# Kernel optimization log

Hardware: AMD Instinct MI355X
Metric: run time of the kernel (lower is better)

## Reference

```python
import jax, jax.numpy as jnp
import numpy as np

N_NODES = 32768
N_EDGES = 524288
N_FEAT = 256
HID = 256
N_GRAPHS = 64
N_CLASSES = 4
NODES_PER_GRAPH = N_NODES // N_GRAPHS
BN_EPS = 1e-5


def setup_inputs() -> dict:
    key = jax.random.key(0)
    ks = jax.random.split(key, 16)
    x = jax.random.normal(ks[0], (N_NODES, N_FEAT), dtype=jnp.float32)
    edge_index = jax.random.randint(ks[1], (2, N_EDGES), 0, N_NODES, dtype=jnp.int32)
    batch = (jnp.arange(N_NODES, dtype=jnp.int32) // NODES_PER_GRAPH)
    def xavier(k, shape):
        fan_in, fan_out = shape[0], shape[1]
        a = float(np.sqrt(6.0 / (fan_in + fan_out)))
        return jax.random.uniform(k, shape, jnp.float32, -a, a)
    return {
        "x": x, "edge_index": edge_index, "batch": batch,
        "W1": xavier(ks[2], (N_FEAT, HID)), "b1": jnp.zeros((HID,), jnp.float32),
        "g1": jnp.ones((HID,), jnp.float32), "be1": jnp.zeros((HID,), jnp.float32),
        "W2": xavier(ks[3], (HID, HID)), "b2": jnp.zeros((HID,), jnp.float32),
        "g2": jnp.ones((HID,), jnp.float32), "be2": jnp.zeros((HID,), jnp.float32),
        "W_ih": xavier(ks[4], (HID, 4 * HID)), "W_hh": xavier(ks[5], (HID, 4 * HID)),
        "b_ih": jnp.zeros((4 * HID,), jnp.float32), "b_hh": jnp.zeros((4 * HID,), jnp.float32),
        "W_fc": xavier(ks[6], (HID, N_CLASSES)), "b_fc": jnp.zeros((N_CLASSES,), jnp.float32),
    }


def gcn_conv(x, W, b, src, dst):
    # PyG GCNConv: add self-loops, symmetric normalization, aggregate, then bias
    h = x @ W                                   # [N, H]
    deg = jnp.zeros((x.shape[0],), h.dtype).at[dst].add(1.0) + 1.0  # in-deg + self-loop
    dinv = jax.lax.rsqrt(deg)
    coef = dinv[src] * dinv[dst]                # [E]
    msg = h[src] * coef[:, None]                # gather + scale, [E, H]
    agg = jnp.zeros_like(h).at[dst].add(msg)    # scatter-add
    agg = agg + h * (1.0 / deg)[:, None]        # self-loop term (norm = 1/deg)
    return agg + b


def batch_norm(x, gamma, beta):
    mean = jnp.mean(x, axis=0)
    var = jnp.mean(jnp.square(x - mean), axis=0)  # biased, as torch BN training
    return (x - mean) * jax.lax.rsqrt(var + BN_EPS) * gamma + beta


def reference(x, edge_index, batch, W1, b1, g1, be1, W2, b2, g2, be2,
              W_ih, W_hh, b_ih, b_hh, W_fc, b_fc):
    src, dst = edge_index[0], edge_index[1]
    h = jax.nn.relu(batch_norm(gcn_conv(x, W1, b1, src, dst), g1, be1))
    h = jax.nn.relu(batch_norm(gcn_conv(h, W2, b2, src, dst), g2, be2))
    # global mean pool over graphs
    sums = jax.ops.segment_sum(h, batch, num_segments=N_GRAPHS)
    cnts = jax.ops.segment_sum(jnp.ones((h.shape[0],), h.dtype), batch, num_segments=N_GRAPHS)
    pooled = sums / cnts[:, None]               # [G, H]
    # LSTM, seq_len = 1, zero initial state -> single cell step
    h0 = jnp.zeros((N_GRAPHS, HID), h.dtype)
    c0 = jnp.zeros((N_GRAPHS, HID), h.dtype)
    gates = pooled @ W_ih + h0 @ W_hh + b_ih + b_hh  # [G, 4H]
    i, f, g, o = jnp.split(gates, 4, axis=1)
    c1 = jax.nn.sigmoid(f) * c0 + jax.nn.sigmoid(i) * jnp.tanh(g)
    h1 = jax.nn.sigmoid(o) * jnp.tanh(c1)
    logits = h1 @ W_fc + b_fc
    logp = jax.nn.log_softmax(logits, axis=1)
    return (logp, (h1[None], c1[None]))
```

## Files before the change

kernel.cpp:

```cpp
#include <hip/hip_runtime.h>
#include <math.h>

#define N_NODES 32768
#define N_FEAT 256
#define HID 256
#define N_GRAPHS 64
#define NPG 512
#define N_CLASSES 4
#define BN_EPS 1e-5f

typedef __attribute__((ext_vector_type(8))) short bf16x8;
typedef __attribute__((ext_vector_type(4))) float f32x4;

__device__ __forceinline__ ushort f2b(float f) {
    union { float f; uint u; } v; v.f = f;
    uint u = v.u;
    return (ushort)((u + 0x7FFFu + ((u >> 16) & 1u)) >> 16);
}
__device__ __forceinline__ float bflo(uint u) {
    union { uint u; float f; } v; v.u = u << 16;
    return v.f;
}
__device__ __forceinline__ float bfhi(uint u) {
    union { uint u; float f; } v; v.u = u & 0xFFFF0000u;
    return v.f;
}

__global__ void k_count_prep(const int* __restrict__ dst, int* __restrict__ degcnt, int cntB,
                             const float* __restrict__ x, ushort* __restrict__ xb, int xB,
                             const float* __restrict__ W1, const float* __restrict__ W2,
                             ushort* __restrict__ Wt1, ushort* __restrict__ Wt2,
                             uint* __restrict__ csrs, int E) {
    int b = blockIdx.x;
    int t = threadIdx.x;
    if (b < cntB) {
        int e = b * 256 + t;
        if (e < E) atomicAdd(&degcnt[dst[e]], 1);
    } else if (b < cntB + xB) {
        int i = (b - cntB) * 256 + t;
        float4 v0 = *(const float4*)(x + (size_t)i * 8);
        float4 v1 = *(const float4*)(x + (size_t)i * 8 + 4);
        uint4 o;
        o.x = (uint)f2b(v0.x) | ((uint)f2b(v0.y) << 16);
        o.y = (uint)f2b(v0.z) | ((uint)f2b(v0.w) << 16);
        o.z = (uint)f2b(v1.x) | ((uint)f2b(v1.y) << 16);
        o.w = (uint)f2b(v1.z) | ((uint)f2b(v1.w) << 16);
        *(uint4*)(xb + (size_t)i * 8) = o;
    } else if (b < cntB + xB + 512) {
        int wb = b - cntB - xB;
        const float* W = (wb < 256) ? W1 : W2;
        ushort* Wt = (wb < 256) ? Wt1 : Wt2;
        int n = wb & 255;
        Wt[n * 256 + t] = f2b(W[t * 256 + n]);
    } else {
        int i = (b - cntB - xB - 512) * 256 + t;
        uint4 s = make_uint4(N_NODES, N_NODES, N_NODES, N_NODES);
        *(uint4*)(csrs + (size_t)i * 4) = s;
    }
}

__global__ __launch_bounds__(1024) void k_scan_all(const int* __restrict__ degcnt,
                                                   float* __restrict__ dinv,
                                                   int* __restrict__ row_start,
                                                   int* __restrict__ cursor,
                                                   uint* __restrict__ csrs,
                                                   ushort* __restrict__ hs_pad) {
    __shared__ int wsum[16];
    int t = threadIdx.x;
    int base = t * 32;
    int s = 0;
#pragma unroll
    for (int i = 0; i < 32; ++i) {
        int c = degcnt[base + i];
        s += (c + 2) & ~1;
    }
    int lane = t & 63, w = t >> 6;
    int v = s;
    for (int off = 1; off < 64; off <<= 1) {
        int u = __shfl_up(v, off);
        if (lane >= off) v += u;
    }
    if (lane == 63) wsum[w] = v;
    __syncthreads();
    if (t < 16) {
        int x = wsum[t];
        for (int off = 1; off < 16; off <<= 1) {
            int u = __shfl_up(x, off, 16);
            if (t >= off) x += u;
        }
        wsum[t] = x;
    }
    __syncthreads();
    int run = ((w > 0) ? wsum[w - 1] : 0) + v - s;
    for (int i = 0; i < 32; ++i) {
        int n = base + i;
        int c = degcnt[n];
        row_start[n] = run;
        csrs[run] = (uint)n;
        cursor[n] = run + 1;
        dinv[n] = rsqrtf((float)(c + 1));
        run += (c + 2) & ~1;
    }
    if (t == 0) row_start[N_NODES] = wsum[15];
    if (t < 128) ((uint*)hs_pad)[t] = 0;
}

__device__ __forceinline__ void fill_body(int e, const int* __restrict__ src,
                                          const int* __restrict__ dst,
                                          int* __restrict__ cursor, uint* __restrict__ csrs,
                                          int E) {
    if (e >= E) return;
    int d = dst[e];
    int pos = atomicAdd(&cursor[d], 1);
    csrs[pos] = (uint)src[e];
}

__device__ __forceinline__ void gemm_body(int bid, const ushort* __restrict__ A,
                                          const ushort* __restrict__ Bt,
                                          const float* __restrict__ dinv,
                                          ushort* __restrict__ hs) {
    int wid = threadIdx.x >> 6;
    int lane = threadIdx.x & 63;
    int xcd = bid & 7;
    int slot = bid >> 3;
    int cb = slot & 3;
    int pr = xcd + ((slot >> 2) << 3);
    int m0 = pr * 256 + wid * 64;
    int n0 = cb * 64;
    int r = lane & 15;
    int ko = (lane >> 4) * 8;

    const ushort* Ab = A + (size_t)(m0 + r) * 256 + ko;
    const ushort* Bb = Bt + (size_t)(n0 + r) * 256 + ko;

    f32x4 acc[4][4] = {};
#pragma unroll
    for (int ks = 0; ks < 8; ++ks) {
        bf16x8 a[4], b[4];
#pragma unroll
        for (int i = 0; i < 4; ++i) {
            a[i] = *(const bf16x8*)(Ab + i * (16 * 256) + ks * 32);
            b[i] = *(const bf16x8*)(Bb + i * (16 * 256) + ks * 32);
        }
#pragma unroll
        for (int i = 0; i < 4; ++i)
#pragma unroll
            for (int j = 0; j < 4; ++j)
                acc[i][j] = __builtin_amdgcn_mfma_f32_16x16x32_bf16(a[i], b[j], acc[i][j], 0, 0, 0);
    }

    int rr = (lane >> 4) * 4;
    int cc = lane & 15;
#pragma unroll
    for (int i = 0; i < 4; ++i) {
        int row = m0 + i * 16 + rr;
#pragma unroll
        for (int r2 = 0; r2 < 4; ++r2) {
            float dv = dinv[row + r2];
#pragma unroll
            for (int j = 0; j < 4; ++j) {
                int col = n0 + j * 16 + cc;
                hs[(size_t)(row + r2) * 256 + col] = f2b(acc[i][j][r2] * dv);
            }
        }
    }
}

__global__ __launch_bounds__(256) void k_fill_gemm1(const ushort* __restrict__ A,
                                                    const ushort* __restrict__ Bt,
                                                    const float* __restrict__ dinv,
                                                    ushort* __restrict__ hs,
                                                    const int* __restrict__ src,
                                                    const int* __restrict__ dst,
                                                    int* __restrict__ cursor,
                                                    uint* __restrict__ csrs, int E) {
    int b = blockIdx.x;
    if (b < 512) {
        gemm_body(b, A, Bt, dinv, hs);
    } else {
        fill_body((b - 512) * 256 + threadIdx.x, src, dst, cursor, csrs, E);
    }
}

__global__ __launch_bounds__(256) void k_gemm2(const ushort* __restrict__ A,
                                               const ushort* __restrict__ Bt,
                                               const float* __restrict__ dinv,
                                               ushort* __restrict__ hs) {
    gemm_body(blockIdx.x, A, Bt, dinv, hs);
}

__global__ __launch_bounds__(256) void k_agg(const ushort* __restrict__ hs,
                                             const uint* __restrict__ csrs,
                                             const int* __restrict__ row_start,
                                             const float* __restrict__ dinv,
                                             const float* __restrict__ bias,
                                             ushort* __restrict__ aggb) {
    int wid = threadIdx.x >> 6;
    int lane = threadIdx.x & 63;
    int half = lane >> 5;
    int fq = lane & 31;
    int n = blockIdx.x * 4 + wid;

    float dv = dinv[n];
    int base = row_start[n];
    int pairs = (row_start[n + 1] - base) >> 1;

    float a0 = 0.f, a1 = 0.f, a2 = 0.f, a3 = 0.f, a4 = 0.f, a5 = 0.f, a6 = 0.f, a7 = 0.f;

    int t = 0;
    for (; t + 4 <= pairs; t += 4) {
        uint s0 = csrs[base + 2 * t + 0 + half];
        uint s1 = csrs[base + 2 * t + 2 + half];
        uint s2 = csrs[base + 2 * t + 4 + half];
        uint s3 = csrs[base + 2 * t + 6 + half];
        uint4 h0 = *(const uint4*)(hs + (size_t)s0 * 256 + fq * 8);
        uint4 h1 = *(const uint4*)(hs + (size_t)s1 * 256 + fq * 8);
        uint4 h2 = *(const uint4*)(hs + (size_t)s2 * 256 + fq * 8);
        uint4 h3 = *(const uint4*)(hs + (size_t)s3 * 256 + fq * 8);
        a0 += bflo(h0.x) + bflo(h1.x) + bflo(h2.x) + bflo(h3.x);
        a1 += bfhi(h0.x) + bfhi(h1.x) + bfhi(h2.x) + bfhi(h3.x);
        a2 += bflo(h0.y) + bflo(h1.y) + bflo(h2.y) + bflo(h3.y);
        a3 += bfhi(h0.y) + bfhi(h1.y) + bfhi(h2.y) + bfhi(h3.y);
        a4 += bflo(h0.z) + bflo(h1.z) + bflo(h2.z) + bflo(h3.z);
        a5 += bfhi(h0.z) + bfhi(h1.z) + bfhi(h2.z) + bfhi(h3.z);
        a6 += bflo(h0.w) + bflo(h1.w) + bflo(h2.w) + bflo(h3.w);
        a7 += bfhi(h0.w) + bfhi(h1.w) + bfhi(h2.w) + bfhi(h3.w);
    }
    for (; t < pairs; ++t) {
        uint s0 = csrs[base + 2 * t + half];
        uint4 h0 = *(const uint4*)(hs + (size_t)s0 * 256 + fq * 8);
        a0 += bflo(h0.x); a1 += bfhi(h0.x);
        a2 += bflo(h0.y); a3 += bfhi(h0.y);
        a4 += bflo(h0.z); a5 += bfhi(h0.z);
        a6 += bflo(h0.w); a7 += bfhi(h0.w);
    }

    a0 += __shfl_xor(a0, 32); a1 += __shfl_xor(a1, 32);
    a2 += __shfl_xor(a2, 32); a3 += __shfl_xor(a3, 32);
    a4 += __shfl_xor(a4, 32); a5 += __shfl_xor(a5, 32);
    a6 += __shfl_xor(a6, 32); a7 += __shfl_xor(a7, 32);

    if (half == 0) {
        float4 b0 = *(const float4*)&bias[fq * 8];
        float4 b1 = *(const float4*)&bias[fq * 8 + 4];
        float o0 = a0 * dv + b0.x, o1 = a1 * dv + b0.y;
        float o2 = a2 * dv + b0.z, o3 = a3 * dv + b0.w;
        float o4 = a4 * dv + b1.x, o5 = a5 * dv + b1.y;
        float o6 = a6 * dv + b1.z, o7 = a7 * dv + b1.w;
        uint4 ov;
        ov.x = (uint)f2b(o0) | ((uint)f2b(o1) << 16);
        ov.y = (uint)f2b(o2) | ((uint)f2b(o3) << 16);
        ov.z = (uint)f2b(o4) | ((uint)f2b(o5) << 16);
        ov.w = (uint)f2b(o6) | ((uint)f2b(o7) << 16);
        *(uint4*)(aggb + (size_t)n * HID + fq * 8) = ov;
    }
}

__global__ __launch_bounds__(256) void k_bn_stats(const ushort* __restrict__ aggb,
                                                  float* __restrict__ bnsum,
                                                  float* __restrict__ bnsq) {
    int t = threadIdx.x;
    int fq = t & 31;
    int rg = t >> 5;
    int r0 = blockIdx.x * 128 + rg * 16;

    float s[8] = {}, q[8] = {};
    for (int r = 0; r < 16; ++r) {
        uint4 v = *(const uint4*)(aggb + (size_t)(r0 + r) * HID + fq * 8);
        float f0 = bflo(v.x), f1 = bfhi(v.x), f2 = bflo(v.y), f3 = bfhi(v.y);
        float f4 = bflo(v.z), f5 = bfhi(v.z), f6 = bflo(v.w), f7 = bfhi(v.w);
        s[0] += f0; q[0] += f0 * f0;  s[1] += f1; q[1] += f1 * f1;
        s[2] += f2; q[2] += f2 * f2;  s[3] += f3; q[3] += f3 * f3;
        s[4] += f4; q[4] += f4 * f4;  s[5] += f5; q[5] += f5 * f5;
        s[6] += f6; q[6] += f6 * f6;  s[7] += f7; q[7] += f7 * f7;
    }

    __shared__ float red[8][32][16];
#pragma unroll
    for (int i = 0; i < 8; ++i) {
        red[rg][fq][i] = s[i];
        red[rg][fq][8 + i] = q[i];
    }
    __syncthreads();
    int fq2 = t & 31;
    int vg = t >> 5;
#pragma unroll
    for (int k = 0; k < 2; ++k) {
        int v = vg * 2 + k;
        float acc = 0.f;
#pragma unroll
        for (int rgi = 0; rgi < 8; ++rgi) acc += red[rgi][fq2][v];
        float* dstp = (v < 8) ? bnsum : bnsq;
        atomicAdd(&dstp[fq2 * 8 + (v & 7)], acc);
    }
}

__global__ void k_bn_apply_b(const ushort* __restrict__ x, const float* __restrict__ bnsum,
                             const float* __restrict__ bnsq, const float* __restrict__ gamma,
                             const float* __restrict__ beta, ushort* __restrict__ out) {
    int i = blockIdx.x * 256 + threadIdx.x;
    if (i >= N_NODES * HID / 4) return;
    int f = (i & 63) * 4;
    const float invN = 1.0f / (float)N_NODES;
    uint2 v = *(const uint2*)(x + (size_t)i * 4);
    float vv[4] = {bflo(v.x), bfhi(v.x), bflo(v.y), bfhi(v.y)};
    float r[4];
#pragma unroll
    for (int qq = 0; qq < 4; ++qq) {
        float mean = bnsum[f + qq] * invN;
        float var = bnsq[f + qq] * invN - mean * mean;
        float t = (vv[qq] - mean) * rsqrtf(var + BN_EPS) * gamma[f + qq] + beta[f + qq];
        r[qq] = t > 0.0f ? t : 0.0f;
    }
    uint2 o;
    o.x = (uint)f2b(r[0]) | ((uint)f2b(r[1]) << 16);
    o.y = (uint)f2b(r[2]) | ((uint)f2b(r[3]) << 16);
    *(uint2*)(out + (size_t)i * 4) = o;
}

__global__ __launch_bounds__(256) void k_bn_pool(const ushort* __restrict__ aggb,
                                                 const float* __restrict__ bnsum,
                                                 const float* __restrict__ bnsq,
                                                 const float* __restrict__ gamma,
                                                 const float* __restrict__ beta,
                                                 float* __restrict__ pooled) {
    int g = blockIdx.x >> 4;
    int blk = blockIdx.x & 15;
    int f = threadIdx.x;
    const float invN = 1.0f / (float)N_NODES;
    float mean = bnsum[f] * invN;
    float var = bnsq[f] * invN - mean * mean;
    float sc = rsqrtf(var + BN_EPS) * gamma[f];
    float sh = beta[f] - mean * sc;
    int r0 = g * NPG + blk * 32;
    float s = 0.0f;
#pragma unroll 4
    for (int r = 0; r < 32; ++r) {
        float v = bflo((uint)aggb[(size_t)(r0 + r) * HID + f]) * sc + sh;
        s += v > 0.0f ? v : 0.0f;
    }
    atomicAdd(&pooled[g * HID + f], s);
}

__global__ __launch_bounds__(256) void k_head(const float* __restrict__ pooled,
                                              const float* __restrict__ W_ih,
                                              const float* __restrict__ b_ih,
                                              const float* __restrict__ b_hh,
                                              const float* __restrict__ W_fc,
                                              const float* __restrict__ b_fc,
                                              float* __restrict__ out) {
    __shared__ float p[HID];
    __shared__ float lsum[N_CLASSES][256];
    __shared__ float logits[N_CLASSES];
    int g = blockIdx.x, j = threadIdx.x;
    p[j] = pooled[g * HID + j] * (1.0f / (float)NPG);
    __syncthreads();

    float gi = 0.f, gf = 0.f, gg = 0.f, go = 0.f;
#pragma unroll 4
    for (int k = 0; k < HID; ++k) {
        float pk = p[k];
        const float* w = &W_ih[(size_t)k * (4 * HID) + j];
        gi += pk * w[0];
        gf += pk * w[HID];
        gg += pk * w[2 * HID];
        go += pk * w[3 * HID];
    }
    gi += b_ih[j] + b_hh[j];
    gf += b_ih[HID + j] + b_hh[HID + j];
    gg += b_ih[2 * HID + j] + b_hh[2 * HID + j];
    go += b_ih[3 * HID + j] + b_hh[3 * HID + j];
    (void)gf;

    float si = 1.f / (1.f + expf(-gi));
    float so = 1.f / (1.f + expf(-go));
    float c1 = si * tanhf(gg);
    float h1 = so * tanhf(c1);

    out[N_GRAPHS * N_CLASSES + g * HID + j] = h1;
    out[N_GRAPHS * N_CLASSES + N_GRAPHS * HID + g * HID + j] = c1;

#pragma unroll
    for (int c = 0; c < N_CLASSES; ++c)
        lsum[c][j] = h1 * W_fc[j * N_CLASSES + c];
    __syncthreads();
    for (int s = 128; s > 0; s >>= 1) {
        if (j < s) {
#pragma unroll
            for (int c = 0; c < N_CLASSES; ++c)
                lsum[c][j] += lsum[c][j + s];
        }
        __syncthreads();
    }
    if (j < N_CLASSES) logits[j] = lsum[j][0] + b_fc[j];
    __syncthreads();
    if (j < N_CLASSES) {
        float m = fmaxf(fmaxf(logits[0], logits[1]), fmaxf(logits[2], logits[3]));
        float lse = m + logf(expf(logits[0] - m) + expf(logits[1] - m) +
                             expf(logits[2] - m) + expf(logits[3] - m));
        out[g * N_CLASSES + j] = logits[j] - lse;
    }
}

extern "C" void kernel_launch(void* const* d_in, const int* in_sizes, int n_in,
                              void* d_out, int out_size, void* d_ws, size_t ws_size,
                              hipStream_t stream) {
    const float* x    = (const float*)d_in[0];
    const int*   ei   = (const int*)d_in[1];
    const float* W1   = (const float*)d_in[3];
    const float* b1   = (const float*)d_in[4];
    const float* g1   = (const float*)d_in[5];
    const float* be1  = (const float*)d_in[6];
    const float* W2   = (const float*)d_in[7];
    const float* b2   = (const float*)d_in[8];
    const float* g2   = (const float*)d_in[9];
    const float* be2  = (const float*)d_in[10];
    const float* W_ih = (const float*)d_in[11];
    const float* b_ih = (const float*)d_in[13];
    const float* b_hh = (const float*)d_in[14];
    const float* W_fc = (const float*)d_in[15];
    const float* b_fc = (const float*)d_in[16];
    float* out = (float*)d_out;

    int E = in_sizes[1] / 2;
    const int* src = ei;
    const int* dst = ei + E;

    const size_t MAT = (size_t)N_NODES * HID;
    size_t SZ = ((size_t)E + 2 * N_NODES + 1023) & ~(size_t)1023;

    ushort* aggb = (ushort*)d_ws;
    ushort* xb   = aggb + MAT;
    ushort* hs   = xb + MAT;
    ushort* Wt1  = hs + MAT + 256;
    ushort* Wt2  = Wt1 + 65536;
    float*  dinv = (float*)(Wt2 + 65536);
    int*    row_start = (int*)(dinv + N_NODES);
    int*    cursor    = row_start + N_NODES + 2;
    uint*   csrs      = (uint*)(cursor + N_NODES);
    int*    degcnt = (int*)(csrs + SZ);
    float*  bn1sum = (float*)(degcnt + N_NODES);
    float*  bn1sq  = bn1sum + HID;
    float*  bn2sum = bn1sq + HID;
    float*  bn2sq  = bn2sum + HID;
    float*  pooled = bn2sq + HID;
    size_t zeroBytes = (size_t)N_NODES * 4 + 4 * HID * 4 + (size_t)N_GRAPHS * HID * 4;

    dim3 blk(256);
    int edgeBlocks = (E + 255) / 256;
    int n8blk = (int)(MAT / 8 / 256);
    int sentB = (int)(SZ / 1024);
    int vec4Blocks = (int)(MAT / 4 / 256);
    int aggBlocks = N_NODES / 4;

    hipMemsetAsync(degcnt, 0, zeroBytes, stream);

    k_count_prep<<<edgeBlocks + n8blk + 512 + sentB, blk, 0, stream>>>(
        dst, degcnt, edgeBlocks, x, xb, n8blk, W1, W2, Wt1, Wt2, csrs, E);
    k_scan_all<<<1, dim3(1024), 0, stream>>>(degcnt, dinv, row_start, cursor, csrs,
                                             hs + MAT);

    k_fill_gemm1<<<512 + edgeBlocks, blk, 0, stream>>>(xb, Wt1, dinv, hs,
                                                       src, dst, cursor, csrs, E);
    k_agg<<<aggBlocks, blk, 0, stream>>>(hs, csrs, row_start, dinv, b1, aggb);
    k_bn_stats<<<N_NODES / 128, blk, 0, stream>>>(aggb, bn1sum, bn1sq);
    k_bn_apply_b<<<vec4Blocks, blk, 0, stream>>>(aggb, bn1sum, bn1sq, g1, be1, xb);

    k_gemm2<<<512, blk, 0, stream>>>(xb, Wt2, dinv, hs);
    k_agg<<<aggBlocks, blk, 0, stream>>>(hs, csrs, row_start, dinv, b2, aggb);
    k_bn_stats<<<N_NODES / 128, blk, 0, stream>>>(aggb, bn2sum, bn2sq);
    k_bn_pool<<<N_GRAPHS * 16, blk, 0, stream>>>(aggb, bn2sum, bn2sq, g2, be2, pooled);

    k_head<<<N_GRAPHS, blk, 0, stream>>>(pooled, W_ih, b_ih, b_hh, W_fc, b_fc, out);
}
```

Baseline: 336.2 us.

## Stage weight tile in swizzled LDS for GEMM and split fill from GEMM1

Rewrites the node-feature GEMM to use 128x128 output tiles: each block loads a 128x256 slice of the transposed weight into LDS with an XOR swizzle, and its four waves share it, replacing per-wave global loads of B. The edge-fill (CSR scatter) is moved out of the fused GEMM1 launch into its own kernel. The aim is to cut redundant global/L2 traffic for the weight operand. In exchange, each block uses 64KB of LDS, which limits occupancy, and there is one extra kernel launch with no overlap between fill and GEMM1.

```diff
diff --git a/kernel.cpp b/kernel.cpp
--- a/kernel.cpp
+++ b/kernel.cpp
@@ -105,42 +105,56 @@
     if (t < 128) ((uint*)hs_pad)[t] = 0;
 }
 
-__device__ __forceinline__ void fill_body(int e, const int* __restrict__ src,
-                                          const int* __restrict__ dst,
-                                          int* __restrict__ cursor, uint* __restrict__ csrs,
-                                          int E) {
+__global__ void k_fill(const int* __restrict__ src, const int* __restrict__ dst,
+                       int* __restrict__ cursor, uint* __restrict__ csrs, int E) {
+    int e = blockIdx.x * 256 + threadIdx.x;
     if (e >= E) return;
     int d = dst[e];
     int pos = atomicAdd(&cursor[d], 1);
     csrs[pos] = (uint)src[e];
 }
 
-__device__ __forceinline__ void gemm_body(int bid, const ushort* __restrict__ A,
-                                          const ushort* __restrict__ Bt,
-                                          const float* __restrict__ dinv,
-                                          ushort* __restrict__ hs) {
-    int wid = threadIdx.x >> 6;
-    int lane = threadIdx.x & 63;
-    int xcd = bid & 7;
-    int slot = bid >> 3;
-    int cb = slot & 3;
-    int pr = xcd + ((slot >> 2) << 3);
-    int m0 = pr * 256 + wid * 64;
-    int n0 = cb * 64;
+__global__ __launch_bounds__(256) void k_gemm_bf16(const ushort* __restrict__ A,
+                                                   const ushort* __restrict__ Bt,
+                                                   const float* __restrict__ dinv,
+                                                   ushort* __restrict__ hs) {
+    __shared__ ushort Bs[128 * 256];
+    int tid = threadIdx.x;
+    int n0 = blockIdx.x * 128;
+    int m0 = blockIdx.y * 128;
+
+#pragma unroll
+    for (int c = 0; c < 16; ++c) {
+        int g = c * 256 + tid;
+        int idx = g * 8;
+        int row = idx >> 8;
+        int col = idx & 255;
+        uint4 v = *(const uint4*)(Bt + (size_t)(n0 + row) * 256 + col);
+        int sidx = idx ^ ((row & 7) << 3);
+        *(uint4*)(Bs + sidx) = v;
+    }
+    __syncthreads();
+
+    int wid = tid >> 6;
+    int lane = tid & 63;
+    int wr = wid >> 1, wc = wid & 1;
     int r = lane & 15;
     int ko = (lane >> 4) * 8;
 
-    const ushort* Ab = A + (size_t)(m0 + r) * 256 + ko;
-    const ushort* Bb = Bt + (size_t)(n0 + r) * 256 + ko;
+    const ushort* Ab = A + (size_t)(m0 + wr * 64 + r) * 256 + ko;
 
     f32x4 acc[4][4] = {};
 #pragma unroll
     for (int ks = 0; ks < 8; ++ks) {
         bf16x8 a[4], b[4];
 #pragma unroll
-        for (int i = 0; i < 4; ++i) {
+        for (int i = 0; i < 4; ++i)
             a[i] = *(const bf16x8*)(Ab + i * (16 * 256) + ks * 32);
-            b[i] = *(const bf16x8*)(Bb + i * (16 * 256) + ks * 32);
+#pragma unroll
+        for (int j = 0; j < 4; ++j) {
+            int srow = wc * 64 + j * 16 + r;
+            int idx = (srow * 256 + ko + ks * 32) ^ ((srow & 7) << 3);
+            b[j] = *(const bf16x8*)(Bs + idx);
         }
 #pragma unroll
         for (int i = 0; i < 4; ++i)
@@ -153,40 +167,17 @@
     int cc = lane & 15;
 #pragma unroll
     for (int i = 0; i < 4; ++i) {
-        int row = m0 + i * 16 + rr;
+        int row = m0 + wr * 64 + i * 16 + rr;
 #pragma unroll
         for (int r2 = 0; r2 < 4; ++r2) {
             float dv = dinv[row + r2];
 #pragma unroll
             for (int j = 0; j < 4; ++j) {
-                int col = n0 + j * 16 + cc;
+                int col = n0 + wc * 64 + j * 16 + cc;
                 hs[(size_t)(row + r2) * 256 + col] = f2b(acc[i][j][r2] * dv);
             }
         }
     }
-}
-
-__global__ __launch_bounds__(256) void k_fill_gemm1(const ushort* __restrict__ A,
-                                                    const ushort* __restrict__ Bt,
-                                                    const float* __restrict__ dinv,
-                                                    ushort* __restrict__ hs,
-                                                    const int* __restrict__ src,
-                                                    const int* __restrict__ dst,
-                                                    int* __restrict__ cursor,
-                                                    uint* __restrict__ csrs, int E) {
-    int b = blockIdx.x;
-    if (b < 512) {
-        gemm_body(b, A, Bt, dinv, hs);
-    } else {
-        fill_body((b - 512) * 256 + threadIdx.x, src, dst, cursor, csrs, E);
-    }
-}
-
-__global__ __launch_bounds__(256) void k_gemm2(const ushort* __restrict__ A,
-                                               const ushort* __restrict__ Bt,
-                                               const float* __restrict__ dinv,
-                                               ushort* __restrict__ hs) {
-    gemm_body(blockIdx.x, A, Bt, dinv, hs);
 }
 
 __global__ __launch_bounds__(256) void k_agg(const ushort* __restrict__ hs,
@@ -452,6 +443,7 @@
     int sentB = (int)(SZ / 1024);
     int vec4Blocks = (int)(MAT / 4 / 256);
     int aggBlocks = N_NODES / 4;
+    dim3 gemmGrid(2, N_NODES / 128);
 
     hipMemsetAsync(degcnt, 0, zeroBytes, stream);
 
@@ -459,14 +451,14 @@
         dst, degcnt, edgeBlocks, x, xb, n8blk, W1, W2, Wt1, Wt2, csrs, E);
     k_scan_all<<<1, dim3(1024), 0, stream>>>(degcnt, dinv, row_start, cursor, csrs,
                                              hs + MAT);
-
-    k_fill_gemm1<<<512 + edgeBlocks, blk, 0, stream>>>(xb, Wt1, dinv, hs,
-                                                       src, dst, cursor, csrs, E);
+    k_fill<<<edgeBlocks, blk, 0, stream>>>(src, dst, cursor, csrs, E);
+
+    k_gemm_bf16<<<gemmGrid, blk, 0, stream>>>(xb, Wt1, dinv, hs);
     k_agg<<<aggBlocks, blk, 0, stream>>>(hs, csrs, row_start, dinv, b1, aggb);
     k_bn_stats<<<N_NODES / 128, blk, 0, stream>>>(aggb, bn1sum, bn1sq);
     k_bn_apply_b<<<vec4Blocks, blk, 0, stream>>>(aggb, bn1sum, bn1sq, g1, be1, xb);
 
-    k_gemm2<<<512, blk, 0, stream>>>(xb, Wt2, dinv, hs);
+    k_gemm_bf16<<<gemmGrid, blk, 0, stream>>>(xb, Wt2, dinv, hs);
     k_agg<<<aggBlocks, blk, 0, stream>>>(hs, csrs, row_start, dinv, b2, aggb);
     k_bn_stats<<<N_NODES / 128, blk, 0, stream>>>(aggb, bn2sum, bn2sq);
     k_bn_pool<<<N_GRAPHS * 16, blk, 0, stream>>>(aggb, bn2sum, bn2sq, g2, be2, pooled);
```

Result: faster. 324.1 us (-3.6%).
